# Performance work log

Hardware: AMD Instinct MI355X
Metric: run time of the kernel (lower is better)

The kernel has to match this reference:

```python
import jax, jax.numpy as jnp
import numpy as np

EMBED_DIM = 1024
NUM_HEADS = 16
RANK = 32
HEAD_DIM = EMBED_DIM // NUM_HEADS
SCALE = 1.0 / np.sqrt(RANK).astype(np.float32)


def setup_inputs() -> dict:
    key = jax.random.key(0)
    ks = jax.random.split(key, 9)
    B, S = 2, 2048
    def lin(k, fan_in, fan_out):
        bound = 1.0 / np.sqrt(fan_in)
        return jax.random.uniform(k, (fan_in, fan_out), jnp.float32, -bound, bound)
    return {
        "hidden_states": jax.random.normal(ks[0], (B, S, EMBED_DIM), jnp.float32),
        "Wq": lin(ks[1], EMBED_DIM, RANK * NUM_HEADS),
        "bq": jnp.zeros((RANK * NUM_HEADS,), jnp.float32),
        "Wk": lin(ks[2], EMBED_DIM, RANK * NUM_HEADS),
        "bk": jnp.zeros((RANK * NUM_HEADS,), jnp.float32),
        "Wv": lin(ks[3], EMBED_DIM, EMBED_DIM),
        "bv": jnp.zeros((EMBED_DIM,), jnp.float32),
        "Wo": lin(ks[4], EMBED_DIM, EMBED_DIM),
        "bo": jnp.zeros((EMBED_DIM,), jnp.float32),
    }


def reference(hidden_states, Wq, bq, Wk, bk, Wv, bv, Wo, bo):
    B, S, E = hidden_states.shape
    q = (hidden_states @ Wq + bq).reshape(B, S, NUM_HEADS, RANK)      # [b,i,h,r]
    k = (hidden_states @ Wk + bk).reshape(B, S, NUM_HEADS, RANK)      # [b,j,h,r]
    v = (hidden_states @ Wv + bv).reshape(B, S, NUM_HEADS, HEAD_DIM)  # [b,j,h,d]
    # full [b,i,j,h] score tensor, softmax over j (axis=2), as in the torch code
    scores = jnp.einsum('bihr,bjhr->bijh', q, k) * SCALE
    attn = jax.nn.softmax(scores, axis=2)
    out = jnp.einsum('bijh,bjhd->bihd', attn, v).reshape(B, S, E)
    return out @ Wo + bo
```

## Files before the change

### kernel.cpp

```cpp
#include <hip/hip_runtime.h>

#define EMBED   1024
#define NHEADS  16
#define RANK    32
#define HDIM    64
#define BATCH   2
#define SEQ     2048
#define BSQ     (BATCH * SEQ)
#define CEXP    0.25505998f

typedef __attribute__((ext_vector_type(8))) short bf16x8;
typedef __attribute__((ext_vector_type(4))) float f32x4;

__device__ __forceinline__ float bf2f(unsigned short u) {
    union { unsigned int i; float f; } x; x.i = ((unsigned int)u) << 16;
    return x.f;
}
__device__ __forceinline__ unsigned short f2bf(float f) {
    union { float f; unsigned int i; } x; x.f = f;
    unsigned int r = x.i + 0x7FFFu + ((x.i >> 16) & 1u);
    return (unsigned short)(r >> 16);
}

#define ASYNC16(gp, lp) \
    __builtin_amdgcn_global_load_lds( \
        (const __attribute__((address_space(1))) void*)(gp), \
        (__attribute__((address_space(3))) void*)(lp), 16, 0, 0)

#define VMDRAIN() asm volatile("s_waitcnt vmcnt(0)" ::: "memory")

__global__ __launch_bounds__(256) void prep_all(
    const float* __restrict__ hs,
    const float* __restrict__ Wq, const float* __restrict__ Wk,
    const float* __restrict__ Wv, const float* __restrict__ Wo,
    const float* __restrict__ bq, const float* __restrict__ bk,
    const float* __restrict__ bv,
    unsigned short* __restrict__ hsb, unsigned short* __restrict__ wT_all,
    unsigned short* __restrict__ woT, float* __restrict__ ball)
{
    __shared__ float L[64][65];
    const int blk = blockIdx.x;
    const int t = threadIdx.x;

    if (blk < 2048) {
        const size_t i = ((size_t)blk * 256 + t) * 8;
        float4 v0 = *(const float4*)(hs + i);
        float4 v1 = *(const float4*)(hs + i + 4);
        ushort4 o0, o1;
        o0.x = f2bf(v0.x); o0.y = f2bf(v0.y); o0.z = f2bf(v0.z); o0.w = f2bf(v0.w);
        o1.x = f2bf(v1.x); o1.y = f2bf(v1.y); o1.z = f2bf(v1.z); o1.w = f2bf(v1.w);
        *(ushort4*)(hsb + i) = o0;
        *(ushort4*)(hsb + i + 4) = o1;
        return;
    }
    if (blk < 2816) {
        int idx = blk - 2048;
        int z, bx, by;
        if (idx < 256) { z = idx >> 7; int r2 = idx & 127; bx = r2 & 7; by = r2 >> 3; }
        else { idx -= 256; z = 2 + (idx >> 8); int r2 = idx & 255; bx = r2 & 15; by = r2 >> 4; }
        const int Nw = (z < 2) ? 512 : 1024;
        const float* W = (z == 0) ? Wq : (z == 1) ? Wk : (z == 2) ? Wv : Wo;
        unsigned short* dst = (z == 3) ? woT : (wT_all + (size_t)z * 512 * 1024);

        const int r = t >> 2, c0 = (t & 3) * 16;
        const float* src = W + (size_t)(by * 64 + r) * Nw + bx * 64 + c0;
        #pragma unroll
        for (int u = 0; u < 4; u++)
            *(float4*)&L[r][c0 + 4 * u] = *(const float4*)(src + 4 * u);
        __syncthreads();
        unsigned short* drow = dst + (size_t)(bx * 64 + r) * 1024 + by * 64 + c0;
        #pragma unroll
        for (int u4 = 0; u4 < 4; u4++) {
            ushort4 o;
            o.x = f2bf(L[c0 + 4 * u4 + 0][r]);
            o.y = f2bf(L[c0 + 4 * u4 + 1][r]);
            o.z = f2bf(L[c0 + 4 * u4 + 2][r]);
            o.w = f2bf(L[c0 + 4 * u4 + 3][r]);
            *(ushort4*)(drow + 4 * u4) = o;
        }
        return;
    }
    {
        const int i = (blk - 2816) * 256 + t;
        ball[i] = (i < 512) ? bq[i] : (i < 1024) ? bk[i - 512] : bv[i - 1024];
    }
}

__global__ __launch_bounds__(256) void gemm_qkv(
    const unsigned short* __restrict__ A, const unsigned short* __restrict__ BT,
    const float* __restrict__ bias,
    unsigned short* __restrict__ qH, unsigned short* __restrict__ kH,
    unsigned short* __restrict__ vTout)
{
    __shared__ unsigned short As[2 * 128 * 32];
    __shared__ unsigned short Bs[2 * 128 * 32];
    const int K = 1024;
    const int t = threadIdx.x;
    const int lane = t & 63;
    const int li = lane & 15, la = lane >> 4;
    const int w = t >> 6, wm = w >> 1, wn = w & 1;
    const int row0 = blockIdx.y * 128, col0 = blockIdx.x * 128;

    const int sr = lane >> 2, sc2 = (lane & 3) * 8;
    const unsigned short* ag = A + (size_t)(row0 + sr) * K + sc2;
    const unsigned short* bg = BT + (size_t)(col0 + sr) * K + sc2;

    f32x4 acc[4][4];
    #pragma unroll
    for (int i = 0; i < 4; i++)
        #pragma unroll
        for (int j = 0; j < 4; j++)
            acc[i][j] = (f32x4){0.f, 0.f, 0.f, 0.f};

    for (int k0 = 0; k0 < K; k0 += 64) {
        #pragma unroll
        for (int kh = 0; kh < 2; kh++)
            #pragma unroll
            for (int u = 0; u < 2; u++) {
                const int ro = w * 32 + u * 16;
                ASYNC16(ag + (size_t)ro * K + k0 + kh * 32, &As[kh * 4096 + ro * 32]);
                ASYNC16(bg + (size_t)ro * K + k0 + kh * 32, &Bs[kh * 4096 + ro * 32]);
            }
        __syncthreads();
        #pragma unroll
        for (int kh = 0; kh < 2; kh++) {
            bf16x8 af[4], bfr[4];
            #pragma unroll
            for (int mt = 0; mt < 4; mt++)
                af[mt] = *(const bf16x8*)&As[kh * 4096 + (wm * 64 + mt * 16 + li) * 32 + la * 8];
            #pragma unroll
            for (int nt = 0; nt < 4; nt++)
                bfr[nt] = *(const bf16x8*)&Bs[kh * 4096 + (wn * 64 + nt * 16 + li) * 32 + la * 8];
            #pragma unroll
            for (int mt = 0; mt < 4; mt++)
                #pragma unroll
                for (int nt = 0; nt < 4; nt++)
                    acc[mt][nt] = __builtin_amdgcn_mfma_f32_16x16x32_bf16(af[mt], bfr[nt], acc[mt][nt], 0, 0, 0);
        }
        __syncthreads();
    }

    const int bb = row0 >> 11;
    const int jb = (row0 & 2047) + wm * 64;
    #pragma unroll
    for (int nt = 0; nt < 4; nt++) {
        const int col = col0 + wn * 64 + nt * 16 + li;
        const float bval = bias[col];
        if (col < 1024) {
            const int hh = (col & 511) >> 5;
            const int rr = col & 31;
            unsigned short* base = ((col < 512) ? qH : kH)
                + ((size_t)(bb * 16 + hh) * 2048) * 32 + rr;
            #pragma unroll
            for (int mt = 0; mt < 4; mt++)
                #pragma unroll
                for (int r = 0; r < 4; r++)
                    base[(size_t)(jb + mt * 16 + la * 4 + r) * 32] =
                        f2bf(acc[mt][nt][r] + bval);
        } else {
            const int hd = col - 1024;
            unsigned short* dcol = vTout + ((size_t)(bb * 16 + (hd >> 6)) * 64 + (hd & 63)) * SEQ;
            #pragma unroll
            for (int mt = 0; mt < 4; mt++) {
                const int srow = jb + mt * 16 + la * 4;
                ushort4 o;
                o.x = f2bf(acc[mt][nt][0] + bval);
                o.y = f2bf(acc[mt][nt][1] + bval);
                o.z = f2bf(acc[mt][nt][2] + bval);
                o.w = f2bf(acc[mt][nt][3] + bval);
                *(ushort4*)(dcol + srow) = o;
            }
        }
    }
}

__global__ __launch_bounds__(256) void gemm_out(
    const unsigned short* __restrict__ A, const unsigned short* __restrict__ BT,
    const float* __restrict__ bias, float* __restrict__ C)
{
    __shared__ unsigned short As[2 * 64 * 32];
    __shared__ unsigned short Bs[2 * 128 * 32];
    const int K = 1024;
    const int t = threadIdx.x;
    const int lane = t & 63;
    const int li = lane & 15, la = lane >> 4;
    const int w = t >> 6, wm = w >> 1, wn = w & 1;
    const int row0 = blockIdx.y * 64, col0 = blockIdx.x * 128;

    const int sr = lane >> 2, sc2 = (lane & 3) * 8;
    const unsigned short* ag = A + (size_t)(row0 + sr) * K + sc2;
    const unsigned short* bg = BT + (size_t)(col0 + sr) * K + sc2;

    f32x4 acc[2][4];
    #pragma unroll
    for (int i = 0; i < 2; i++)
        #pragma unroll
        for (int j = 0; j < 4; j++)
            acc[i][j] = (f32x4){0.f, 0.f, 0.f, 0.f};

    for (int k0 = 0; k0 < K; k0 += 64) {
        #pragma unroll
        for (int kh = 0; kh < 2; kh++) {
            ASYNC16(ag + (size_t)(w * 16) * K + k0 + kh * 32, &As[kh * 2048 + (w * 16) * 32]);
            #pragma unroll
            for (int u = 0; u < 2; u++) {
                const int ro = w * 32 + u * 16;
                ASYNC16(bg + (size_t)ro * K + k0 + kh * 32, &Bs[kh * 4096 + ro * 32]);
            }
        }
        __syncthreads();
        #pragma unroll
        for (int kh = 0; kh < 2; kh++) {
            bf16x8 af[2], bfr[4];
            #pragma unroll
            for (int mt = 0; mt < 2; mt++)
                af[mt] = *(const bf16x8*)&As[kh * 2048 + (wm * 32 + mt * 16 + li) * 32 + la * 8];
            #pragma unroll
            for (int nt = 0; nt < 4; nt++)
                bfr[nt] = *(const bf16x8*)&Bs[kh * 4096 + (wn * 64 + nt * 16 + li) * 32 + la * 8];
            #pragma unroll
            for (int mt = 0; mt < 2; mt++)
                #pragma unroll
                for (int nt = 0; nt < 4; nt++)
                    acc[mt][nt] = __builtin_amdgcn_mfma_f32_16x16x32_bf16(af[mt], bfr[nt], acc[mt][nt], 0, 0, 0);
        }
        __syncthreads();
    }

    #pragma unroll
    for (int nt = 0; nt < 4; nt++) {
        const int col = col0 + wn * 64 + nt * 16 + li;
        const float bval = bias[col];
        #pragma unroll
        for (int mt = 0; mt < 2; mt++)
            #pragma unroll
            for (int r = 0; r < 4; r++) {
                const int row = row0 + wm * 32 + mt * 16 + la * 4 + r;
                C[(size_t)row * 1024 + col] = acc[mt][nt][r] + bval;
            }
    }
}

__global__ __launch_bounds__(128) void attn_v12(
    const unsigned short* __restrict__ qH,
    const unsigned short* __restrict__ kH,
    const unsigned short* __restrict__ vT,
    unsigned short* __restrict__ ao)
{
    __shared__ unsigned short kt[2][64 * 32];
    __shared__ unsigned short vt[2][64 * 64];
    __shared__ unsigned short P[64 * 72];

    const int t = threadIdx.x;
    const int lane = t & 63;
    const int li = lane & 15, la = lane >> 4;
    const int w = t >> 6;

    const int bh = blockIdx.x & 31;
    const int itile = blockIdx.x >> 5;
    const int i0 = itile * 64;
    const int b = bh >> 4, h = bh & 15;

    bf16x8 qf[2];
    #pragma unroll
    for (int iq = 0; iq < 2; iq++) {
        const unsigned short* qp = qH + ((size_t)bh * 2048 + i0 + w * 32 + iq * 16 + li) * 32 + la * 8;
        ushort4 q0 = *(const ushort4*)qp;
        ushort4 q1 = *(const ushort4*)(qp + 4);
        short u[8];
        u[0] = (short)f2bf(bf2f(q0.x) * CEXP);
        u[1] = (short)f2bf(bf2f(q0.y) * CEXP);
        u[2] = (short)f2bf(bf2f(q0.z) * CEXP);
        u[3] = (short)f2bf(bf2f(q0.w) * CEXP);
        u[4] = (short)f2bf(bf2f(q1.x) * CEXP);
        u[5] = (short)f2bf(bf2f(q1.y) * CEXP);
        u[6] = (short)f2bf(bf2f(q1.z) * CEXP);
        u[7] = (short)f2bf(bf2f(q1.w) * CEXP);
        qf[iq] = *(const bf16x8*)u;
    }

    bf16x8 vones;
    #pragma unroll
    for (int u2 = 0; u2 < 8; u2++) vones[u2] = (short)0x3F80;

    const int cK8 = ((lane & 3) ^ ((lane >> 3) & 3)) * 8;
    const unsigned short* kpt = kH + (size_t)bh * 2048 * 32
                               + (size_t)(w * 32 + (lane >> 2)) * 32 + cK8;
    const int rV = lane >> 3;
    const int cV8 = ((lane & 7) ^ rV) * 8;
    const unsigned short* vpt = vT + ((size_t)bh * 64 + w * 32 + rV) * SEQ + cV8;

    const int kcol  = (la ^ ((li >> 1) & 3)) * 8;
    const int vcol0 = ((0 * 4 + la) ^ (li & 7)) * 8;
    const int vcol1 = ((1 * 4 + la) ^ (li & 7)) * 8;

    f32x4 accO[2][4], accl[2];
    #pragma unroll
    for (int iq = 0; iq < 2; iq++) {
        accl[iq] = (f32x4){0.f, 0.f, 0.f, 0.f};
        #pragma unroll
        for (int dt = 0; dt < 4; dt++) accO[iq][dt] = (f32x4){0.f, 0.f, 0.f, 0.f};
    }
    const int prow0 = w * 32 + li;
    const int prow1 = prow0 + 16;

    ASYNC16(kpt,            &kt[0][(w * 32) * 32]);
    ASYNC16(kpt + 16 * 32,  &kt[0][(w * 32 + 16) * 32]);
    #pragma unroll
    for (int q = 0; q < 4; q++)
        ASYNC16(vpt + (size_t)q * 8 * SEQ, &vt[0][(w * 32 + q * 8) * 64]);

    #define ATTN_BODY(BUF, OTHER, JPRE)                                            \
    {                                                                              \
        VMDRAIN();                                                                 \
        __syncthreads();                                                           \
        const int jn = (JPRE) & 2047;                                              \
        ASYNC16(kpt + (size_t)jn * 32,           &kt[OTHER][(w * 32) * 32]);       \
        ASYNC16(kpt + (size_t)jn * 32 + 16 * 32, &kt[OTHER][(w * 32 + 16) * 32]);  \
        _Pragma("unroll")                                                          \
        for (int q = 0; q < 4; q++)                                                \
            ASYNC16(vpt + jn + (size_t)q * 8 * SEQ, &vt[OTHER][(w * 32 + q * 8) * 64]); \
        bf16x8 kf[4];                                                              \
        _Pragma("unroll")                                                          \
        for (int jt = 0; jt < 4; jt++)                                             \
            kf[jt] = *(const bf16x8*)&kt[BUF][(jt * 16 + li) * 32 + kcol];         \
        f32x4 sc0[4], sc1[4];                                                      \
        _Pragma("unroll")                                                          \
        for (int jt = 0; jt < 4; jt++) {                                           \
            sc0[jt] = __builtin_amdgcn_mfma_f32_16x16x32_bf16(kf[jt], qf[0], (f32x4){0.f,0.f,0.f,0.f}, 0, 0, 0); \
            sc1[jt] = __builtin_amdgcn_mfma_f32_16x16x32_bf16(kf[jt], qf[1], (f32x4){0.f,0.f,0.f,0.f}, 0, 0, 0); \
        }                                                                          \
        _Pragma("unroll")                                                          \
        for (int jt = 0; jt < 4; jt++) {                                           \
            float e0 = __builtin_amdgcn_exp2f(sc0[jt][0]);                         \
            float e1 = __builtin_amdgcn_exp2f(sc0[jt][1]);                         \
            float e2 = __builtin_amdgcn_exp2f(sc0[jt][2]);                         \
            float e3 = __builtin_amdgcn_exp2f(sc0[jt][3]);                         \
            uint2 pk;                                                              \
            asm("v_cvt_pk_bf16_f32 %0, %1, %2" : "=v"(pk.x) : "v"(e0), "v"(e1));   \
            asm("v_cvt_pk_bf16_f32 %0, %1, %2" : "=v"(pk.y) : "v"(e2), "v"(e3));   \
            *(uint2*)&P[prow0 * 72 + jt * 16 + la * 4] = pk;                       \
        }                                                                          \
        _Pragma("unroll")                                                          \
        for (int jt = 0; jt < 4; jt++) {                                           \
            float e0 = __builtin_amdgcn_exp2f(sc1[jt][0]);                         \
            float e1 = __builtin_amdgcn_exp2f(sc1[jt][1]);                         \
            float e2 = __builtin_amdgcn_exp2f(sc1[jt][2]);                         \
            float e3 = __builtin_amdgcn_exp2f(sc1[jt][3]);                         \
            uint2 pk;                                                              \
            asm("v_cvt_pk_bf16_f32 %0, %1, %2" : "=v"(pk.x) : "v"(e0), "v"(e1));   \
            asm("v_cvt_pk_bf16_f32 %0, %1, %2" : "=v"(pk.y) : "v"(e2), "v"(e3));   \
            *(uint2*)&P[prow1 * 72 + jt * 16 + la * 4] = pk;                       \
        }                                                                          \
        _Pragma("unroll")                                                          \
        for (int ks = 0; ks < 2; ks++) {                                           \
            const bf16x8 pf0 = *(const bf16x8*)&P[prow0 * 72 + ks * 32 + la * 8];  \
            const bf16x8 pf1 = *(const bf16x8*)&P[prow1 * 72 + ks * 32 + la * 8];  \
            accl[0] = __builtin_amdgcn_mfma_f32_16x16x32_bf16(pf0, vones, accl[0], 0, 0, 0); \
            accl[1] = __builtin_amdgcn_mfma_f32_16x16x32_bf16(pf1, vones, accl[1], 0, 0, 0); \
            const int vcol = ks ? vcol1 : vcol0;                                   \
            _Pragma("unroll")                                                      \
            for (int dt = 0; dt < 4; dt++) {                                       \
                const bf16x8 vf = *(const bf16x8*)&vt[BUF][(dt * 16 + li) * 64 + vcol]; \
                accO[0][dt] = __builtin_amdgcn_mfma_f32_16x16x32_bf16(pf0, vf, accO[0][dt], 0, 0, 0); \
                accO[1][dt] = __builtin_amdgcn_mfma_f32_16x16x32_bf16(pf1, vf, accO[1][dt], 0, 0, 0); \
            }                                                                      \
        }                                                                          \
    }

    for (int j0 = 0; j0 < SEQ; j0 += 128) {
        ATTN_BODY(0, 1, j0 + 64)
        ATTN_BODY(1, 0, j0 + 128)
    }
    #undef ATTN_BODY

    VMDRAIN();
    __syncthreads();

    #pragma unroll
    for (int iq = 0; iq < 2; iq++) {
        float linv[4];
        #pragma unroll
        for (int r = 0; r < 4; r++) linv[r] = 1.f / accl[iq][r];
        #pragma unroll
        for (int dt = 0; dt < 4; dt++)
            #pragma unroll
            for (int r = 0; r < 4; r++) {
                const int row = b * SEQ + i0 + w * 32 + iq * 16 + la * 4 + r;
                ao[(size_t)row * 1024 + h * 64 + dt * 16 + li] = f2bf(accO[iq][dt][r] * linv[r]);
            }
    }
}

extern "C" void kernel_launch(void* const* d_in, const int* in_sizes, int n_in,
                              void* d_out, int out_size, void* d_ws, size_t ws_size,
                              hipStream_t stream) {
    const float* hs = (const float*)d_in[0];
    const float* Wq = (const float*)d_in[1];
    const float* bq = (const float*)d_in[2];
    const float* Wk = (const float*)d_in[3];
    const float* bk = (const float*)d_in[4];
    const float* Wv = (const float*)d_in[5];
    const float* bv = (const float*)d_in[6];
    const float* Wo = (const float*)d_in[7];
    const float* bo = (const float*)d_in[8];

    char* p = (char*)d_ws;
    unsigned short* hsb = (unsigned short*)(p);
    unsigned short* wT  = (unsigned short*)(p + 8388608u);
    unsigned short* woT = (unsigned short*)(p + 12582912u);
    float*          ball= (float*)(p + 14680064u);
    unsigned short* qHb = (unsigned short*)(p + 14688256u);
    unsigned short* kHb = (unsigned short*)(p + 18882560u);
    unsigned short* vTb = (unsigned short*)(p + 23076864u);
    unsigned short* ao  = (unsigned short*)(p + 31465472u);

    prep_all<<<dim3(2824), 256, 0, stream>>>(hs, Wq, Wk, Wv, Wo, bq, bk, bv,
                                             hsb, wT, woT, ball);

    gemm_qkv<<<dim3(16, 32), 256, 0, stream>>>(hsb, wT, ball, qHb, kHb, vTb);

    attn_v12<<<dim3(1024), 128, 0, stream>>>(qHb, kHb, vTb, ao);

    gemm_out<<<dim3(8, 64), 256, 0, stream>>>(ao, woT, bo, (float*)d_out);
}
```

Baseline: 178.6 us.

## Load K/V fragments directly into registers with register double buffering

The attention kernel stops staging K and V tiles through double-buffered LDS with async global-to-LDS copies, barriers and vmcnt drains. Each wave now loads its MFMA K and V fragments straight from global memory into registers, prefetching the next 64-key tile while the current one is computed. This removes block-wide synchronisation and LDS traffic for K/V. In exchange both waves fetch the same K/V data, doubling cache traffic, and the extra fragment registers may lower occupancy.

```diff
diff --git a/kernel.cpp b/kernel.cpp
--- a/kernel.cpp
+++ b/kernel.cpp
@@ -26,8 +26,6 @@
     __builtin_amdgcn_global_load_lds( \
         (const __attribute__((address_space(1))) void*)(gp), \
         (__attribute__((address_space(3))) void*)(lp), 16, 0, 0)
-
-#define VMDRAIN() asm volatile("s_waitcnt vmcnt(0)" ::: "memory")
 
 __global__ __launch_bounds__(256) void prep_all(
     const float* __restrict__ hs,
@@ -241,14 +239,12 @@
     }
 }
 
-__global__ __launch_bounds__(128) void attn_v12(
+__global__ __launch_bounds__(128) void attn_v13(
     const unsigned short* __restrict__ qH,
     const unsigned short* __restrict__ kH,
     const unsigned short* __restrict__ vT,
     unsigned short* __restrict__ ao)
 {
-    __shared__ unsigned short kt[2][64 * 32];
-    __shared__ unsigned short vt[2][64 * 64];
     __shared__ unsigned short P[64 * 72];
 
     const int t = threadIdx.x;
@@ -283,16 +279,8 @@
     #pragma unroll
     for (int u2 = 0; u2 < 8; u2++) vones[u2] = (short)0x3F80;
 
-    const int cK8 = ((lane & 3) ^ ((lane >> 3) & 3)) * 8;
-    const unsigned short* kpt = kH + (size_t)bh * 2048 * 32
-                               + (size_t)(w * 32 + (lane >> 2)) * 32 + cK8;
-    const int rV = lane >> 3;
-    const int cV8 = ((lane & 7) ^ rV) * 8;
-    const unsigned short* vpt = vT + ((size_t)bh * 64 + w * 32 + rV) * SEQ + cV8;
-
-    const int kcol  = (la ^ ((li >> 1) & 3)) * 8;
-    const int vcol0 = ((0 * 4 + la) ^ (li & 7)) * 8;
-    const int vcol1 = ((1 * 4 + la) ^ (li & 7)) * 8;
+    const unsigned short* kL = kH + (size_t)bh * 2048 * 32 + (size_t)li * 32 + la * 8;
+    const unsigned short* vL = vT + (size_t)bh * 64 * SEQ + (size_t)li * SEQ + la * 8;
 
     f32x4 accO[2][4], accl[2];
     #pragma unroll
@@ -304,31 +292,25 @@
     const int prow0 = w * 32 + li;
     const int prow1 = prow0 + 16;
 
-    ASYNC16(kpt,            &kt[0][(w * 32) * 32]);
-    ASYNC16(kpt + 16 * 32,  &kt[0][(w * 32 + 16) * 32]);
-    #pragma unroll
-    for (int q = 0; q < 4; q++)
-        ASYNC16(vpt + (size_t)q * 8 * SEQ, &vt[0][(w * 32 + q * 8) * 64]);
-
-    #define ATTN_BODY(BUF, OTHER, JPRE)                                            \
+    #define LOADK(dst, J)                                                          \
+    { _Pragma("unroll")                                                            \
+      for (int jt = 0; jt < 4; jt++)                                               \
+          dst[jt] = *(const bf16x8*)(kL + (size_t)((J) + jt * 16) * 32); }
+
+    #define LOADV(dst, J)                                                          \
+    { _Pragma("unroll")                                                            \
+      for (int dt = 0; dt < 4; dt++)                                               \
+          _Pragma("unroll")                                                        \
+          for (int ks = 0; ks < 2; ks++)                                           \
+              dst[dt * 2 + ks] = *(const bf16x8*)(vL + (size_t)(dt * 16) * SEQ + (J) + ks * 32); }
+
+    #define ATTN_BODY(KF, VF)                                                      \
     {                                                                              \
-        VMDRAIN();                                                                 \
-        __syncthreads();                                                           \
-        const int jn = (JPRE) & 2047;                                              \
-        ASYNC16(kpt + (size_t)jn * 32,           &kt[OTHER][(w * 32) * 32]);       \
-        ASYNC16(kpt + (size_t)jn * 32 + 16 * 32, &kt[OTHER][(w * 32 + 16) * 32]);  \
-        _Pragma("unroll")                                                          \
-        for (int q = 0; q < 4; q++)                                                \
-            ASYNC16(vpt + jn + (size_t)q * 8 * SEQ, &vt[OTHER][(w * 32 + q * 8) * 64]); \
-        bf16x8 kf[4];                                                              \
-        _Pragma("unroll")                                                          \
-        for (int jt = 0; jt < 4; jt++)                                             \
-            kf[jt] = *(const bf16x8*)&kt[BUF][(jt * 16 + li) * 32 + kcol];         \
         f32x4 sc0[4], sc1[4];                                                      \
         _Pragma("unroll")                                                          \
         for (int jt = 0; jt < 4; jt++) {                                           \
-            sc0[jt] = __builtin_amdgcn_mfma_f32_16x16x32_bf16(kf[jt], qf[0], (f32x4){0.f,0.f,0.f,0.f}, 0, 0, 0); \
-            sc1[jt] = __builtin_amdgcn_mfma_f32_16x16x32_bf16(kf[jt], qf[1], (f32x4){0.f,0.f,0.f,0.f}, 0, 0, 0); \
+            sc0[jt] = __builtin_amdgcn_mfma_f32_16x16x32_bf16(KF[jt], qf[0], (f32x4){0.f,0.f,0.f,0.f}, 0, 0, 0); \
+            sc1[jt] = __builtin_amdgcn_mfma_f32_16x16x32_bf16(KF[jt], qf[1], (f32x4){0.f,0.f,0.f,0.f}, 0, 0, 0); \
         }                                                                          \
         _Pragma("unroll")                                                          \
         for (int jt = 0; jt < 4; jt++) {                                           \
@@ -358,24 +340,29 @@
             const bf16x8 pf1 = *(const bf16x8*)&P[prow1 * 72 + ks * 32 + la * 8];  \
             accl[0] = __builtin_amdgcn_mfma_f32_16x16x32_bf16(pf0, vones, accl[0], 0, 0, 0); \
             accl[1] = __builtin_amdgcn_mfma_f32_16x16x32_bf16(pf1, vones, accl[1], 0, 0, 0); \
-            const int vcol = ks ? vcol1 : vcol0;                                   \
             _Pragma("unroll")                                                      \
             for (int dt = 0; dt < 4; dt++) {                                       \
-                const bf16x8 vf = *(const bf16x8*)&vt[BUF][(dt * 16 + li) * 64 + vcol]; \
-                accO[0][dt] = __builtin_amdgcn_mfma_f32_16x16x32_bf16(pf0, vf, accO[0][dt], 0, 0, 0); \
-                accO[1][dt] = __builtin_amdgcn_mfma_f32_16x16x32_bf16(pf1, vf, accO[1][dt], 0, 0, 0); \
+                accO[0][dt] = __builtin_amdgcn_mfma_f32_16x16x32_bf16(pf0, VF[dt * 2 + ks], accO[0][dt], 0, 0, 0); \
+                accO[1][dt] = __builtin_amdgcn_mfma_f32_16x16x32_bf16(pf1, VF[dt * 2 + ks], accO[1][dt], 0, 0, 0); \
             }                                                                      \
         }                                                                          \
     }
 
+    bf16x8 kfA[4], vfA[8], kfB[4], vfB[8];
+    LOADK(kfA, 0)
+    LOADV(vfA, 0)
     for (int j0 = 0; j0 < SEQ; j0 += 128) {
-        ATTN_BODY(0, 1, j0 + 64)
-        ATTN_BODY(1, 0, j0 + 128)
+        LOADK(kfB, j0 + 64)
+        LOADV(vfB, j0 + 64)
+        ATTN_BODY(kfA, vfA)
+        const int jn = (j0 + 128) & 2047;
+        LOADK(kfA, jn)
+        LOADV(vfA, jn)
+        ATTN_BODY(kfB, vfB)
     }
     #undef ATTN_BODY
-
-    VMDRAIN();
-    __syncthreads();
+    #undef LOADK
+    #undef LOADV
 
     #pragma unroll
     for (int iq = 0; iq < 2; iq++) {
@@ -420,7 +407,7 @@
 
     gemm_qkv<<<dim3(16, 32), 256, 0, stream>>>(hsb, wT, ball, qHb, kHb, vTb);
 
-    attn_v12<<<dim3(1024), 128, 0, stream>>>(qHb, kHb, vTb, ao);
+    attn_v13<<<dim3(1024), 128, 0, stream>>>(qHb, kHb, vTb, ao);
 
     gemm_out<<<dim3(8, 64), 256, 0, stream>>>(ao, woT, bo, (float*)d_out);
 }
```

New measurement: 210.4 us. 17.8% more time.
